# Optimization experiments

Measured on AMD Instinct MI355X. Metric: run time of the kernel, lower is better.

Reference implementation:

```python
import jax, jax.numpy as jnp
import numpy as np
import math

B, S, D = 2, 1024, 512
H = 8
DH = D // H
N_NEURONS = 512
K = 16
N_BASIS = 8
RANK = 64
D_FF = 2048
LN_EPS = 1e-5


def _layer_norm(x, g, b):
    mu = jnp.mean(x, axis=-1, keepdims=True)
    var = jnp.var(x, axis=-1, keepdims=True)
    return (x - mu) * jax.lax.rsqrt(var + LN_EPS) * g + b


def setup_inputs() -> dict:
    key = jax.random.key(0)
    ks = jax.random.split(key, 16)
    x = jax.random.normal(ks[0], (B, S, D), dtype=jnp.float32)
    # causal mask [B,1,S,S] (True = keep)
    mask = jnp.broadcast_to(jnp.tril(jnp.ones((S, S), dtype=bool)), (B, 1, S, S))
    inp = {
        "x": x,
        "neuron_emb": jax.random.normal(ks[1], (N_NEURONS, D)) * 0.02,
        "Wq": jax.random.normal(ks[2], (D, D)) * 0.02, "bq": jnp.zeros((D,)),
        "Wk": jax.random.normal(ks[3], (D, D)) * 0.02, "bk": jnp.zeros((D,)),
        "Wv": jax.random.normal(ks[4], (D, D)) * 0.02, "bv": jnp.zeros((D,)),
        "Wg": jax.random.normal(ks[5], (2 * D, 2)) * 0.02, "bg": jnp.zeros((2,)),
        "basis_A": jax.random.normal(ks[6], (N_BASIS, D, RANK)) * 0.05,
        "basis_B": jax.random.normal(ks[7], (N_BASIS, RANK, D_FF)) * 0.05,
        "neuron_coords": jax.random.normal(ks[8], (N_NEURONS, N_BASIS)) * 0.5,
        "Wd": jax.random.normal(ks[9], (D_FF, D)) * 0.02, "bd": jnp.zeros((D,)),
        "ln1_g": jnp.ones((D,)), "ln1_b": jnp.zeros((D,)),
        "ln2_g": jnp.ones((D,)), "ln2_b": jnp.zeros((D,)),
        "mask": mask,
    }
    return inp


def reference(x, neuron_emb, Wq, bq, Wk, bk, Wv, bv, Wg, bg, basis_A, basis_B,
              neuron_coords, Wd, bd, ln1_g, ln1_b, ln2_g, ln2_b, mask):
    normed = _layer_norm(x, ln1_g, ln1_b)
    # --- router: cross-attention context ---
    q = (normed @ Wq + bq).reshape(B, S, H, DH).transpose(0, 2, 1, 3)
    k = (normed @ Wk + bk).reshape(B, S, H, DH).transpose(0, 2, 1, 3)
    v = (normed @ Wv + bv).reshape(B, S, H, DH).transpose(0, 2, 1, 3)
    attn = jnp.einsum('bhsd,bhtd->bhst', q, k) / math.sqrt(DH)
    attn = jnp.where(mask, attn, -jnp.inf)
    attn = jax.nn.softmax(attn, axis=-1)
    context = jnp.einsum('bhst,bhtd->bhsd', attn, v)
    context = context.transpose(0, 2, 1, 3).reshape(B, S, D)
    # --- gated neuron scoring + top-k ---
    token_scores = normed @ neuron_emb.T            # [B,S,N]
    context_scores = context @ neuron_emb.T         # [B,S,N]
    gate = jax.nn.softmax(jnp.concatenate([normed, context], axis=-1) @ Wg + bg, axis=-1)
    scores = gate[:, :, 0:1] * token_scores + gate[:, :, 1:2] * context_scores
    topk_scores, topk_idx = jax.lax.top_k(scores, K)  # [B,S,K]
    weights = jax.nn.softmax(topk_scores, axis=-1)
    # --- neuron info residual ---
    neuron_info = jnp.einsum('bsk,bskd->bsd', weights, neuron_emb[topk_idx])
    x = x + neuron_info
    # --- per-token basis-mixed low-rank FFN ---
    normed2 = _layer_norm(x, ln2_g, ln2_b)
    coords = neuron_coords[topk_idx]                # [B,S,K,n_basis]
    token_coords = jnp.einsum('bsk,bskn->bsn', weights, coords)  # [B,S,n_basis]
    # h = x @ (sum_n c_n A_n): contract without materializing [B,S,D,R]
    h = jnp.einsum('bsnr,bsn->bsr', jnp.einsum('bsd,ndr->bsnr', normed2, basis_A), token_coords)
    h = jnp.einsum('bsnf,bsn->bsf', jnp.einsum('bsr,nrf->bsnf', h, basis_B), token_coords)
    h = jax.nn.gelu(h, approximate=False)
    out = h @ Wd + bd
    x = x + out
    return (x, topk_idx)
```

## Files before the change

kernel.cpp:

```cpp
#include <hip/hip_runtime.h>
#include <hip/hip_bf16.h>

#define Bv 2
#define Sv 1024
#define Dv 512
#define Hv 8
#define Nv 512
#define Kv 16
#define NBv 8
#define DFv 2048
#define NTOK (Bv*Sv)

typedef __attribute__((ext_vector_type(8))) short short8;
typedef __attribute__((ext_vector_type(4))) float float4v;

__launch_bounds__(256)
__global__ void ln64_k(const float* __restrict__ x, const float* __restrict__ g,
                       const float* __restrict__ b, double* __restrict__ out)
{
    const int t = blockIdx.x;
    const size_t base = (size_t)t * Dv;
    const int tid = threadIdx.x;
    double v0 = (double)x[base + tid];
    double v1 = (double)x[base + tid + 256];
    double s = v0 + v1, ss = v0 * v0 + v1 * v1;
    #pragma unroll
    for (int off = 32; off; off >>= 1) { s += __shfl_xor(s, off); ss += __shfl_xor(ss, off); }
    __shared__ double red[4][2];
    const int wv = tid >> 6, ln = tid & 63;
    if (ln == 0) { red[wv][0] = s; red[wv][1] = ss; }
    __syncthreads();
    s  = red[0][0] + red[1][0] + red[2][0] + red[3][0];
    ss = red[0][1] + red[1][1] + red[2][1] + red[3][1];
    double mu  = s * (1.0 / Dv);
    double var = ss * (1.0 / Dv) - mu * mu;
    double rstd = 1.0 / sqrt(var + 1e-5);
    out[base + tid]       = (v0 - mu) * rstd * (double)g[tid]       + (double)b[tid];
    out[base + tid + 256] = (v1 - mu) * rstd * (double)g[tid + 256] + (double)b[tid + 256];
}

__launch_bounds__(256)
__global__ void qkv64_k(const double* __restrict__ A,
                        const float* __restrict__ Wq, const float* __restrict__ Wk,
                        const float* __restrict__ Wv, const float* __restrict__ bq,
                        const float* __restrict__ bk, const float* __restrict__ bvv,
                        double* __restrict__ qo, double* __restrict__ ko,
                        double* __restrict__ vo)
{
    const int z = blockIdx.z;
    const float* Bm  = (z == 0) ? Wq : (z == 1) ? Wk : Wv;
    const float* bia = (z == 0) ? bq : (z == 1) ? bk : bvv;
    double* Cout     = (z == 0) ? qo : (z == 1) ? ko : vo;
    const int N = Dv, Kd = Dv;
    __shared__ double As[16][68];
    __shared__ double Bs[16][68];
    const int tid = threadIdx.x;
    const int m0 = blockIdx.y * 64, n0 = blockIdx.x * 64;
    const int tx = tid & 15, ty = tid >> 4;
    double acc[4][4] = {};
    const int lm = tid >> 2, lk4 = (tid & 3) << 2;
    for (int k0 = 0; k0 < Kd; k0 += 16) {
        double4 av = *(const double4*)(A + (size_t)(m0 + lm) * Kd + k0 + lk4);
        As[lk4 + 0][lm] = av.x; As[lk4 + 1][lm] = av.y;
        As[lk4 + 2][lm] = av.z; As[lk4 + 3][lm] = av.w;
        const int kk = tid >> 4, n4 = (tid & 15) << 2;
        float4 bv4 = *(const float4*)(Bm + (size_t)(k0 + kk) * N + n0 + n4);
        Bs[kk][n4 + 0] = (double)bv4.x; Bs[kk][n4 + 1] = (double)bv4.y;
        Bs[kk][n4 + 2] = (double)bv4.z; Bs[kk][n4 + 3] = (double)bv4.w;
        __syncthreads();
        #pragma unroll
        for (int kk2 = 0; kk2 < 16; kk2++) {
            double a_[4], b_[4];
            *(double4*)a_ = *(const double4*)&As[kk2][ty << 2];
            *(double4*)b_ = *(const double4*)&Bs[kk2][tx << 2];
            #pragma unroll
            for (int i = 0; i < 4; i++)
                #pragma unroll
                for (int j = 0; j < 4; j++)
                    acc[i][j] = fma(a_[i], b_[j], acc[i][j]);
        }
        __syncthreads();
    }
    #pragma unroll
    for (int i = 0; i < 4; i++) {
        const int row = m0 + (ty << 2) + i;
        #pragma unroll
        for (int j = 0; j < 4; j++) {
            const int col = n0 + (tx << 2) + j;
            Cout[(size_t)row * N + col] = acc[i][j] + (double)bia[col];
        }
    }
}

__launch_bounds__(256)
__global__ void scores64_k(const double* __restrict__ A0, const double* __restrict__ A1,
                           const double* __restrict__ gate, const float* __restrict__ Bm,
                           double* __restrict__ Cbase)
{
    const int M = NTOK, N = Nv, Kd = Dv;
    const int z = blockIdx.z;
    const int kbeg = z * (Dv / 2), kend = kbeg + Dv / 2;
    double* Cout = Cbase + (size_t)z * M * N;
    __shared__ double As[16][68];
    __shared__ double Bs[16][68];
    const int tid = threadIdx.x;
    const int m0 = blockIdx.y * 64, n0 = blockIdx.x * 64;
    const int tx = tid & 15, ty = tid >> 4;
    double acc[4][4] = {};
    const int lm = tid >> 2, lk4 = (tid & 3) << 2;
    for (int k0 = kbeg; k0 < kend; k0 += 16) {
        const double g0 = gate[2 * (m0 + lm)], g1 = gate[2 * (m0 + lm) + 1];
        double4 a0 = *(const double4*)(A0 + (size_t)(m0 + lm) * Kd + k0 + lk4);
        double4 a1 = *(const double4*)(A1 + (size_t)(m0 + lm) * Kd + k0 + lk4);
        As[lk4 + 0][lm] = g0 * a0.x + g1 * a1.x;
        As[lk4 + 1][lm] = g0 * a0.y + g1 * a1.y;
        As[lk4 + 2][lm] = g0 * a0.z + g1 * a1.z;
        As[lk4 + 3][lm] = g0 * a0.w + g1 * a1.w;
        const int nn = tid >> 2, kq = (tid & 3) << 2;
        float4 bv4 = *(const float4*)(Bm + (size_t)(n0 + nn) * Kd + k0 + kq);
        Bs[kq + 0][nn] = (double)bv4.x; Bs[kq + 1][nn] = (double)bv4.y;
        Bs[kq + 2][nn] = (double)bv4.z; Bs[kq + 3][nn] = (double)bv4.w;
        __syncthreads();
        #pragma unroll
        for (int kk = 0; kk < 16; kk++) {
            double a_[4], b_[4];
            *(double4*)a_ = *(const double4*)&As[kk][ty << 2];
            *(double4*)b_ = *(const double4*)&Bs[kk][tx << 2];
            #pragma unroll
            for (int i = 0; i < 4; i++)
                #pragma unroll
                for (int j = 0; j < 4; j++)
                    acc[i][j] = fma(a_[i], b_[j], acc[i][j]);
        }
        __syncthreads();
    }
    #pragma unroll
    for (int i = 0; i < 4; i++) {
        const int row = m0 + (ty << 2) + i;
        #pragma unroll
        for (int j = 0; j < 4; j++)
            Cout[(size_t)row * N + n0 + (tx << 2) + j] = acc[i][j];
    }
}

template<int EPI>
__launch_bounds__(256)
__global__ void mfma_k(const __hip_bfloat16* __restrict__ A, const __hip_bfloat16* __restrict__ B,
                       void* __restrict__ Cout_, int M, int N, int Kt, int kper)
{
    __shared__ __hip_bfloat16 As[128][40];
    __shared__ __hip_bfloat16 Bs[128][40];
    const int tid = threadIdx.x;
    const int m0 = blockIdx.y * 128, n0 = blockIdx.x * 128;
    const int z = blockIdx.z;
    const int kbeg = z * kper, kend = kbeg + kper;
    const int w = tid >> 6, l = tid & 63;
    const int wr = (w >> 1) * 64, wc = (w & 1) * 64;
    const int lm = l & 15, quad = l >> 4;
    float4v acc[4][4];
    #pragma unroll
    for (int i = 0; i < 4; i++)
        #pragma unroll
        for (int j = 0; j < 4; j++)
            acc[i][j] = (float4v){0.f, 0.f, 0.f, 0.f};
    const int srow = tid >> 1, skb = (tid & 1) * 16;
    for (int k0 = kbeg; k0 < kend; k0 += 32) {
        *(uint4*)&As[srow][skb]     = *(const uint4*)(A + (size_t)(m0 + srow) * Kt + k0 + skb);
        *(uint4*)&As[srow][skb + 8] = *(const uint4*)(A + (size_t)(m0 + srow) * Kt + k0 + skb + 8);
        *(uint4*)&Bs[srow][skb]     = *(const uint4*)(B + (size_t)(n0 + srow) * Kt + k0 + skb);
        *(uint4*)&Bs[srow][skb + 8] = *(const uint4*)(B + (size_t)(n0 + srow) * Kt + k0 + skb + 8);
        __syncthreads();
        short8 af[4], bf[4];
        #pragma unroll
        for (int mi = 0; mi < 4; mi++) af[mi] = *(const short8*)&As[wr + mi * 16 + lm][quad * 8];
        #pragma unroll
        for (int ni = 0; ni < 4; ni++) bf[ni] = *(const short8*)&Bs[wc + ni * 16 + lm][quad * 8];
        #pragma unroll
        for (int mi = 0; mi < 4; mi++)
            #pragma unroll
            for (int ni = 0; ni < 4; ni++)
                acc[mi][ni] = __builtin_amdgcn_mfma_f32_16x16x32_bf16(af[mi], bf[ni], acc[mi][ni], 0, 0, 0);
        __syncthreads();
    }
    #pragma unroll
    for (int mi = 0; mi < 4; mi++) {
        #pragma unroll
        for (int ni = 0; ni < 4; ni++) {
            const int col = n0 + wc + ni * 16 + lm;
            #pragma unroll
            for (int r = 0; r < 4; r++) {
                const int row = m0 + wr + mi * 16 + quad * 4 + r;
                float c = acc[mi][ni][r];
                if (EPI == 0) {
                    ((float*)Cout_)[(size_t)z * M * N + (size_t)row * N + col] = c;
                } else {
                    c = 0.5f * c * (1.0f + erff(c * 0.70710678118654752f));
                    ((__hip_bfloat16*)Cout_)[(size_t)row * N + col] = __float2bfloat16(c);
                }
            }
        }
    }
}

__device__ __constant__ int c_slotbase[4] = {0, 0, 384, 640};
__device__ __constant__ int c_cnt[4]      = {0, 24, 16, 8};

__launch_bounds__(256)
__global__ void attn64c_k(const double* __restrict__ q, const double* __restrict__ k,
                          const double* __restrict__ v, double* __restrict__ ctxun,
                          double* __restrict__ Opart, double* __restrict__ mbuf,
                          double* __restrict__ lbuf)
{
    const int qt = blockIdx.x, bh = blockIdx.y, ch = blockIdx.z;
    if (qt < ch * 8) return;
    const int b = bh >> 3, h = bh & 7;
    __shared__ double Qs[32][70];
    __shared__ double Kt[64][34];
    __shared__ double Vs[32][70];
    const int tid = threadIdx.x;
    const int r = tid >> 3, cc = tid & 7;
    const int lane = tid & 63;
    const int lbase = lane & 56;
    const size_t qoff = ((size_t)b * Sv + (size_t)qt * 32) * Dv + h * 64;
    #pragma unroll
    for (int i = 0; i < 4; i++) {
        int f = i * 256 + tid;
        int row = f >> 5, c2 = (f & 31) * 2;
        *(double2*)&Qs[row][c2] = *(const double2*)(q + qoff + (size_t)row * Dv + c2);
    }
    double O[8] = {};
    double mrun = -1e300, lrun = 0.0;
    const int iglob = qt * 32 + r;
    const int jbeg = ch * 8;
    const int jend = (qt < jbeg + 7) ? qt : (jbeg + 7);
    for (int jt = jbeg; jt <= jend; jt++) {
        __syncthreads();
        const size_t koff = ((size_t)b * Sv + (size_t)jt * 32) * Dv + h * 64;
        #pragma unroll
        for (int i = 0; i < 4; i++) {
            int f = i * 256 + tid;
            int row = f >> 5, c2 = (f & 31) * 2;
            double2 kv = *(const double2*)(k + koff + (size_t)row * Dv + c2);
            Kt[c2][row]     = kv.x;
            Kt[c2 + 1][row] = kv.y;
            *(double2*)&Vs[row][c2] = *(const double2*)(v + koff + (size_t)row * Dv + c2);
        }
        __syncthreads();
        double a[4] = {0.0, 0.0, 0.0, 0.0};
        #pragma unroll 8
        for (int kk = 0; kk < 64; kk += 2) {
            double2 qv  = *(const double2*)&Qs[r][kk];
            double2 ka0 = *(const double2*)&Kt[kk][cc * 4];
            double2 ka1 = *(const double2*)&Kt[kk][cc * 4 + 2];
            double2 kb0 = *(const double2*)&Kt[kk + 1][cc * 4];
            double2 kb1 = *(const double2*)&Kt[kk + 1][cc * 4 + 2];
            a[0] = fma(qv.x, ka0.x, fma(qv.y, kb0.x, a[0]));
            a[1] = fma(qv.x, ka0.y, fma(qv.y, kb0.y, a[1]));
            a[2] = fma(qv.x, ka1.x, fma(qv.y, kb1.x, a[2]));
            a[3] = fma(qv.x, ka1.y, fma(qv.y, kb1.y, a[3]));
        }
        double p[4];
        double mx = -1e300;
        #pragma unroll
        for (int jj = 0; jj < 4; jj++) {
            const int jglob = jt * 32 + cc * 4 + jj;
            p[jj] = (jglob <= iglob) ? a[jj] * 0.125 : -1e300;
            mx = fmax(mx, p[jj]);
        }
        mx = fmax(mx, __shfl_xor(mx, 1));
        mx = fmax(mx, __shfl_xor(mx, 2));
        mx = fmax(mx, __shfl_xor(mx, 4));
        const double mnew = fmax(mrun, mx);
        double rsum = 0.0;
        #pragma unroll
        for (int jj = 0; jj < 4; jj++) { p[jj] = exp(p[jj] - mnew); rsum += p[jj]; }
        rsum += __shfl_xor(rsum, 1);
        rsum += __shfl_xor(rsum, 2);
        rsum += __shfl_xor(rsum, 4);
        const double alpha = exp(mrun - mnew);
        lrun = lrun * alpha + rsum;
        mrun = mnew;
        #pragma unroll
        for (int c = 0; c < 8; c++) O[c] *= alpha;
        #pragma unroll
        for (int jsrc = 0; jsrc < 8; jsrc++) {
            #pragma unroll
            for (int jj = 0; jj < 4; jj++) {
                const double pj = __shfl(p[jj], lbase + jsrc);
                const double* vrow = &Vs[jsrc * 4 + jj][cc * 8];
                #pragma unroll
                for (int c2 = 0; c2 < 8; c2 += 2) {
                    double2 vv = *(const double2*)&vrow[c2];
                    O[c2 + 0] = fma(pj, vv.x, O[c2 + 0]);
                    O[c2 + 1] = fma(pj, vv.y, O[c2 + 1]);
                }
            }
        }
    }
    if (cc == 0) {
        const int mi = ((bh * 32 + qt) * 4 + ch) * 32 + r;
        mbuf[mi] = mrun; lbuf[mi] = lrun;
    }
    if (ch == 0) {
        const size_t obase = ((size_t)b * Sv + (size_t)iglob) * Dv + h * 64 + cc * 8;
        #pragma unroll
        for (int c2 = 0; c2 < 8; c2 += 2) { double2 t{O[c2], O[c2+1]}; *(double2*)(ctxun + obase + c2) = t; }
    } else {
        const int slot = c_slotbase[ch] + bh * c_cnt[ch] + (qt - ch * 8);
        const size_t obase = ((size_t)slot * 32 + r) * 64 + cc * 8;
        #pragma unroll
        for (int c2 = 0; c2 < 8; c2 += 2) { double2 t{O[c2], O[c2+1]}; *(double2*)(Opart + obase + c2) = t; }
    }
}

__launch_bounds__(256)
__global__ void attnmerge_k(double* __restrict__ ctx, const double* __restrict__ Opart,
                            const double* __restrict__ mbuf, const double* __restrict__ lbuf)
{
    const size_t i = (size_t)blockIdx.x * 256 + threadIdx.x;
    const size_t e = i * 2;
    const int d = (int)(e & 511);
    const int s = (int)((e >> 9) & 1023);
    const int b = (int)(e >> 19);
    const int h = d >> 6;
    const int qt = s >> 5, r = s & 31;
    const int bh = b * 8 + h;
    int nch = qt >> 3; if (nch > 3) nch = 3;
    const int mib = ((bh * 32 + qt) * 4) * 32 + r;
    double ms = mbuf[mib];
    for (int c = 1; c <= nch; c++) ms = fmax(ms, mbuf[mib + c * 32]);
    double2 o = *(const double2*)(ctx + e);
    double a0 = exp(mbuf[mib] - ms);
    double den = lbuf[mib] * a0;
    o.x *= a0; o.y *= a0;
    for (int c = 1; c <= nch; c++) {
        const double ac = exp(mbuf[mib + c * 32] - ms);
        den += lbuf[mib + c * 32] * ac;
        const int slot = c_slotbase[c] + bh * c_cnt[c] + (qt - c * 8);
        const size_t op = ((size_t)slot * 32 + r) * 64 + (d & 63);
        double2 oc = *(const double2*)(Opart + op);
        o.x = fma(ac, oc.x, o.x);
        o.y = fma(ac, oc.y, o.y);
    }
    const double inv = 1.0 / den;
    o.x *= inv; o.y *= inv;
    *(double2*)(ctx + e) = o;
}

__launch_bounds__(256)
__global__ void gate64_k(const double* __restrict__ normed, const double* __restrict__ ctx,
                         const float* __restrict__ Wg, const float* __restrict__ bg,
                         double* __restrict__ gate)
{
    const int wv = threadIdx.x >> 6, lane = threadIdx.x & 63;
    const int t = blockIdx.x * 4 + wv;
    double a0 = 0.0, a1 = 0.0;
    for (int d = lane; d < Dv; d += 64) {
        double nv = normed[(size_t)t * Dv + d];
        double cv = ctx[(size_t)t * Dv + d];
        a0 += nv * (double)Wg[2 * d]     + cv * (double)Wg[2 * (d + Dv)];
        a1 += nv * (double)Wg[2 * d + 1] + cv * (double)Wg[2 * (d + Dv) + 1];
    }
    #pragma unroll
    for (int off = 32; off; off >>= 1) { a0 += __shfl_xor(a0, off); a1 += __shfl_xor(a1, off); }
    if (lane == 0) {
        a0 += (double)bg[0]; a1 += (double)bg[1];
        double m = fmax(a0, a1);
        double e0 = exp(a0 - m), e1 = exp(a1 - m);
        double inv = 1.0 / (e0 + e1);
        gate[2 * t] = e0 * inv; gate[2 * t + 1] = e1 * inv;
    }
}

__launch_bounds__(256)
__global__ void topk64_k(const double* __restrict__ s0, const float* __restrict__ x,
                         const float* __restrict__ emb, const float* __restrict__ coords,
                         const float* __restrict__ g2, const float* __restrict__ b2,
                         float* __restrict__ x2, __hip_bfloat16* __restrict__ normed2bf,
                         float* __restrict__ tcoords, float* __restrict__ idx_out)
{
    __shared__ double sc[4][Nv];
    const int wv = threadIdx.x >> 6, lane = threadIdx.x & 63;
    const int t = blockIdx.x * 4 + wv;
    const double* s1 = s0 + (size_t)NTOK * Nv;
    double* s = sc[wv];
    #pragma unroll
    for (int i = 0; i < 8; i++) {
        const size_t idx = (size_t)t * Nv + i * 64 + lane;
        s[i * 64 + lane] = s0[idx] + s1[idx];
    }
    __syncthreads();
    double wval[Kv]; int widx[Kv];
    for (int kk = 0; kk < Kv; kk++) {
        double bvv = -1e300; int bi = Nv;
        #pragma unroll
        for (int i = 0; i < 8; i++) {
            const int d = lane * 8 + i;
            const double vv = s[d];
            if (vv > bvv) { bvv = vv; bi = d; }
        }
        #pragma unroll
        for (int off = 1; off < 64; off <<= 1) {
            double ov = __shfl_xor(bvv, off);
            int    oi = __shfl_xor(bi, off);
            if (ov > bvv || (ov == bvv && oi < bi)) { bvv = ov; bi = oi; }
        }
        wval[kk] = bvv; widx[kk] = bi;
        __syncthreads();
        if (lane == (bi >> 3)) s[bi] = -1e301;
        __syncthreads();
        if (lane == kk) idx_out[(size_t)t * Kv + kk] = (float)bi;
    }
    double w[Kv]; double sum = 0.0;
    #pragma unroll
    for (int kk = 0; kk < Kv; kk++) { w[kk] = exp(wval[kk] - wval[0]); sum += w[kk]; }
    const double invs = 1.0 / sum;
    #pragma unroll
    for (int kk = 0; kk < Kv; kk++) w[kk] *= invs;
    float xv[8];
    float sm = 0.0f, sq = 0.0f;
    #pragma unroll
    for (int i = 0; i < 8; i++) {
        const int d = lane + 64 * i;
        double info = 0.0;
        #pragma unroll
        for (int kk = 0; kk < Kv; kk++)
            info = fma(w[kk], (double)emb[(size_t)widx[kk] * Dv + d], info);
        float vv = (float)((double)x[(size_t)t * Dv + d] + info);
        xv[i] = vv;
        x2[(size_t)t * Dv + d] = vv;
        sm += vv; sq += vv * vv;
    }
    #pragma unroll
    for (int off = 32; off; off >>= 1) { sm += __shfl_xor(sm, off); sq += __shfl_xor(sq, off); }
    const float mu = sm * (1.0f / Dv);
    const float var = sq * (1.0f / Dv) - mu * mu;
    const float rstd = rsqrtf(var + 1e-5f);
    #pragma unroll
    for (int i = 0; i < 8; i++) {
        const int d = lane + 64 * i;
        normed2bf[(size_t)t * Dv + d] = __float2bfloat16((xv[i] - mu) * rstd * g2[d] + b2[d]);
    }
    if (lane < NBv) {
        double tc = 0.0;
        #pragma unroll
        for (int kk = 0; kk < Kv; kk++)
            tc = fma(w[kk], (double)coords[(size_t)widx[kk] * NBv + lane], tc);
        tcoords[t * NBv + lane] = (float)tc;
    }
}

__launch_bounds__(256)
__global__ void acatbf_k(const float* __restrict__ bA, __hip_bfloat16* __restrict__ AcatT)
{
    const int i = blockIdx.x * 256 + threadIdx.x;
    const int d = i & 511, nc = i >> 9;
    const int n = nc >> 6, r = nc & 63;
    AcatT[i] = __float2bfloat16(bA[n * 32768 + d * 64 + r]);
}

__launch_bounds__(256)
__global__ void tr2bf_k(const float* __restrict__ in, __hip_bfloat16* __restrict__ out,
                        int R, int C)
{
    __shared__ float tile[32][33];
    const int c0 = blockIdx.x * 32, r0 = blockIdx.y * 32;
    const int tx = threadIdx.x & 31, ty = threadIdx.x >> 5;
    #pragma unroll
    for (int i = 0; i < 4; i++)
        tile[ty + 8 * i][tx] = in[(size_t)(r0 + ty + 8 * i) * C + c0 + tx];
    __syncthreads();
    #pragma unroll
    for (int i = 0; i < 4; i++)
        out[(size_t)(c0 + ty + 8 * i) * R + r0 + tx] = __float2bfloat16(tile[tx][ty + 8 * i]);
}

__launch_bounds__(256)
__global__ void combine_k(const float* __restrict__ Gp, const float* __restrict__ tcoords,
                          __hip_bfloat16* __restrict__ u_bf)
{
    const size_t M1 = (size_t)NTOK * Dv;
    const int wv = threadIdx.x >> 6, lane = threadIdx.x & 63;
    const int t = blockIdx.x * 4 + wv;
    float cs[NBv];
    #pragma unroll
    for (int n = 0; n < NBv; n++) cs[n] = tcoords[t * NBv + n];
    float h = 0.0f;
    #pragma unroll
    for (int n = 0; n < NBv; n++) {
        const size_t gi = (size_t)t * Dv + n * 64 + lane;
        float g = Gp[gi] + Gp[gi + M1] + Gp[gi + 2 * M1] + Gp[gi + 3 * M1];
        h = fmaf(cs[n], g, h);
    }
    #pragma unroll
    for (int n = 0; n < NBv; n++)
        u_bf[(size_t)t * Dv + n * 64 + lane] = __float2bfloat16(cs[n] * h);
}

__launch_bounds__(256)
__global__ void reduce4_k(const float* __restrict__ p4, const float* __restrict__ bd,
                          const float* __restrict__ x2, float* __restrict__ xout)
{
    const size_t M1 = (size_t)NTOK * Dv;
    const size_t i = (size_t)blockIdx.x * 256 + threadIdx.x;
    float c = p4[i] + p4[i + M1] + p4[i + 2 * M1] + p4[i + 3 * M1];
    xout[i] = c + bd[i & 511] + x2[i];
}

extern "C" void kernel_launch(void* const* d_in, const int* in_sizes, int n_in,
                              void* d_out, int out_size, void* d_ws, size_t ws_size,
                              hipStream_t stream) {
    (void)in_sizes; (void)n_in; (void)out_size; (void)ws_size;
    const size_t M1 = (size_t)NTOK * Dv;

    const float* x   = (const float*)d_in[0];
    const float* emb = (const float*)d_in[1];
    const float* Wq  = (const float*)d_in[2];
    const float* bq  = (const float*)d_in[3];
    const float* Wk  = (const float*)d_in[4];
    const float* bk  = (const float*)d_in[5];
    const float* Wv  = (const float*)d_in[6];
    const float* bvv = (const float*)d_in[7];
    const float* Wg  = (const float*)d_in[8];
    const float* bg  = (const float*)d_in[9];
    const float* bA  = (const float*)d_in[10];
    const float* bB  = (const float*)d_in[11];
    const float* crd = (const float*)d_in[12];
    const float* Wd  = (const float*)d_in[13];
    const float* bd  = (const float*)d_in[14];
    const float* l1g = (const float*)d_in[15];
    const float* l1b = (const float*)d_in[16];
    const float* l2g = (const float*)d_in[17];
    const float* l2b = (const float*)d_in[18];

    double* normed64 = (double*)d_ws;
    double* q64      = normed64 + M1;
    double* k64      = q64 + M1;
    double* v64      = k64 + M1;
    double* ctx64    = v64 + M1;
    double* Opart    = ctx64 + M1;
    double* mbuf     = Opart + 1572864;
    double* lbuf     = mbuf + 65536;
    double* gate64   = lbuf + 65536;
    float*  tcoords  = (float*)(gate64 + 4096);
    __hip_bfloat16* AcatT = (__hip_bfloat16*)(tcoords + 16384);

    double* s0 = q64;
    float*  x2 = (float*)v64;
    __hip_bfloat16* normed2bf = (__hip_bfloat16*)(x2 + M1);
    __hip_bfloat16* u_bf      = normed2bf + M1;
    float* Gp = (float*)q64;
    float* p4 = (float*)q64;
    __hip_bfloat16* hf_bf = (__hip_bfloat16*)Opart;
    __hip_bfloat16* bBT   = hf_bf + 4 * M1;
    __hip_bfloat16* WdT   = bBT + M1;

    float* xout    = (float*)d_out;
    float* idx_out = (float*)d_out + M1;

    ln64_k<<<NTOK, 256, 0, stream>>>(x, l1g, l1b, normed64);
    qkv64_k<<<dim3(8, 32, 3), 256, 0, stream>>>(normed64, Wq, Wk, Wv, bq, bk, bvv, q64, k64, v64);
    attn64c_k<<<dim3(32, 16, 4), 256, 0, stream>>>(q64, k64, v64, ctx64, Opart, mbuf, lbuf);
    attnmerge_k<<<(int)(M1 / 512), 256, 0, stream>>>(ctx64, Opart, mbuf, lbuf);
    gate64_k<<<NTOK / 4, 256, 0, stream>>>(normed64, ctx64, Wg, bg, gate64);
    scores64_k<<<dim3(8, 32, 2), 256, 0, stream>>>(normed64, ctx64, gate64, emb, s0);
    topk64_k<<<NTOK / 4, 256, 0, stream>>>(s0, x, emb, crd, l2g, l2b, x2, normed2bf, tcoords, idx_out);
    acatbf_k<<<1024, 256, 0, stream>>>(bA, AcatT);
    tr2bf_k<<<dim3(DFv / 32, Dv / 32), 256, 0, stream>>>(bB, bBT, Dv, DFv);
    tr2bf_k<<<dim3(Dv / 32, DFv / 32), 256, 0, stream>>>(Wd, WdT, DFv, Dv);
    mfma_k<0><<<dim3(4, 16, 4), 256, 0, stream>>>(normed2bf, AcatT, Gp, NTOK, Dv, Dv, Dv / 4);
    combine_k<<<NTOK / 4, 256, 0, stream>>>(Gp, tcoords, u_bf);
    mfma_k<1><<<dim3(16, 16, 1), 256, 0, stream>>>(u_bf, bBT, hf_bf, NTOK, DFv, Dv, Dv);
    mfma_k<0><<<dim3(4, 16, 4), 256, 0, stream>>>(hf_bf, WdT, p4, NTOK, Dv, DFv, DFv / 4);
    reduce4_k<<<(int)(M1 / 256), 256, 0, stream>>>(p4, bd, x2, xout);
}
```

Baseline: 620.8 us.

## Use FP64 MFMA for fused QKV projection with runtime layout probing

Replaces the scalar-FMA FP64 QKV GEMM (three separate z-slices) with one kernel that computes Q, K and V together from a shared A tile. It uses the 16x16x4 f64 MFMA instruction. The kernel first probes the MFMA operand and output lane layout at runtime with known integer inputs and picks a matching mapping. If no mapping matches, it falls back to a scalar FMA path. This aims to move the FP64 GEMM onto matrix cores and to reuse the A tile across all three weights, at the cost of a small probe per block and extra branching.

```diff
diff --git a/kernel.cpp b/kernel.cpp
--- a/kernel.cpp
+++ b/kernel.cpp
@@ -13,6 +13,7 @@
 
 typedef __attribute__((ext_vector_type(8))) short short8;
 typedef __attribute__((ext_vector_type(4))) float float4v;
+typedef __attribute__((ext_vector_type(4))) double dbl4;
 
 __launch_bounds__(256)
 __global__ void ln64_k(const float* __restrict__ x, const float* __restrict__ g,
@@ -40,54 +41,150 @@
 }
 
 __launch_bounds__(256)
-__global__ void qkv64_k(const double* __restrict__ A,
+__global__ void qkvMC_k(const double* __restrict__ A,
                         const float* __restrict__ Wq, const float* __restrict__ Wk,
                         const float* __restrict__ Wv, const float* __restrict__ bq,
                         const float* __restrict__ bk, const float* __restrict__ bvv,
                         double* __restrict__ qo, double* __restrict__ ko,
                         double* __restrict__ vo)
 {
-    const int z = blockIdx.z;
-    const float* Bm  = (z == 0) ? Wq : (z == 1) ? Wk : Wv;
-    const float* bia = (z == 0) ? bq : (z == 1) ? bk : bvv;
-    double* Cout     = (z == 0) ? qo : (z == 1) ? ko : vo;
-    const int N = Dv, Kd = Dv;
-    __shared__ double As[16][68];
-    __shared__ double Bs[16][68];
+    __shared__ double As[32][18];
+    __shared__ double Bs[3][16][66];
     const int tid = threadIdx.x;
-    const int m0 = blockIdx.y * 64, n0 = blockIdx.x * 64;
-    const int tx = tid & 15, ty = tid >> 4;
-    double acc[4][4] = {};
-    const int lm = tid >> 2, lk4 = (tid & 3) << 2;
-    for (int k0 = 0; k0 < Kd; k0 += 16) {
-        double4 av = *(const double4*)(A + (size_t)(m0 + lm) * Kd + k0 + lk4);
-        As[lk4 + 0][lm] = av.x; As[lk4 + 1][lm] = av.y;
-        As[lk4 + 2][lm] = av.z; As[lk4 + 3][lm] = av.w;
-        const int kk = tid >> 4, n4 = (tid & 15) << 2;
-        float4 bv4 = *(const float4*)(Bm + (size_t)(k0 + kk) * N + n0 + n4);
-        Bs[kk][n4 + 0] = (double)bv4.x; Bs[kk][n4 + 1] = (double)bv4.y;
-        Bs[kk][n4 + 2] = (double)bv4.z; Bs[kk][n4 + 3] = (double)bv4.w;
-        __syncthreads();
-        #pragma unroll
-        for (int kk2 = 0; kk2 < 16; kk2++) {
-            double a_[4], b_[4];
-            *(double4*)a_ = *(const double4*)&As[kk2][ty << 2];
-            *(double4*)b_ = *(const double4*)&Bs[kk2][tx << 2];
-            #pragma unroll
-            for (int i = 0; i < 4; i++)
+    const int n0 = blockIdx.x * 64, m0 = blockIdx.y * 32;
+    const int w = tid >> 6, l = tid & 63;
+    const int mt = (w >> 1) * 16, wc = (w & 1) * 32;
+    const int ar = tid >> 3, ak = (tid & 7) * 2;
+    const int bkk = tid >> 4, bn = (tid & 15) * 4;
+
+    int rA = 0, kA = 0, kB = 0, cB = 0, dsel = -1;
+    #pragma unroll 1
+    for (int ab = 0; ab < 4; ab++) {
+        if (dsel >= 0) break;
+        const int a_ = ab & 1, b_ = ab >> 1;
+        const int rA_ = a_ ? (l >> 2) : (l & 15);
+        const int kA_ = a_ ? (l & 3)  : (l >> 4);
+        const int kB_ = b_ ? (l & 3)  : (l >> 4);
+        const int cB_ = b_ ? (l >> 2) : (l & 15);
+        const double av  = (double)(((rA_ * 37 + kA_ * 11) % 19) + 1);
+        const double bvp = (double)(((kB_ * 23 + cB_ * 7) % 17) + 1);
+        dbl4 dd = __builtin_amdgcn_mfma_f64_16x16x4f64(av, bvp, (dbl4){0.0, 0.0, 0.0, 0.0}, 0, 0, 0);
+        #pragma unroll 1
+        for (int d = 0; d < 4; d++) {
+            if (dsel >= 0) break;
+            int okv = 1;
+            #pragma unroll
+            for (int r = 0; r < 4; r++) {
+                const int i_ = (d == 0) ? 4 * (l >> 4) + r
+                             : (d == 1) ? (l & 15)
+                             : (d == 2) ? (l >> 4) + 4 * r
+                             :            (l & 15);
+                const int j_ = (d == 0) ? (l & 15)
+                             : (d == 1) ? 4 * (l >> 4) + r
+                             : (d == 2) ? (l & 15)
+                             :            (l >> 4) + 4 * r;
+                double e = 0.0;
                 #pragma unroll
-                for (int j = 0; j < 4; j++)
-                    acc[i][j] = fma(a_[i], b_[j], acc[i][j]);
-        }
-        __syncthreads();
-    }
-    #pragma unroll
-    for (int i = 0; i < 4; i++) {
-        const int row = m0 + (ty << 2) + i;
-        #pragma unroll
-        for (int j = 0; j < 4; j++) {
-            const int col = n0 + (tx << 2) + j;
-            Cout[(size_t)row * N + col] = acc[i][j] + (double)bia[col];
+                for (int kk2 = 0; kk2 < 4; kk2++)
+                    e += (double)(((i_ * 37 + kk2 * 11) % 19) + 1)
+                       * (double)(((kk2 * 23 + j_ * 7) % 17) + 1);
+                okv &= (dd[r] == e) ? 1 : 0;
+            }
+            if (__all(okv)) { dsel = d; rA = rA_; kA = kA_; kB = kB_; cB = cB_; }
+        }
+    }
+
+    auto stage = [&](int k0) {
+        double2 avv = *(const double2*)(A + (size_t)(m0 + ar) * Dv + k0 + ak);
+        *(double2*)&As[ar][ak] = avv;
+        {
+            float4 b4 = *(const float4*)(Wq + (size_t)(k0 + bkk) * Dv + n0 + bn);
+            Bs[0][bkk][bn] = (double)b4.x; Bs[0][bkk][bn + 1] = (double)b4.y;
+            Bs[0][bkk][bn + 2] = (double)b4.z; Bs[0][bkk][bn + 3] = (double)b4.w;
+        }
+        {
+            float4 b4 = *(const float4*)(Wk + (size_t)(k0 + bkk) * Dv + n0 + bn);
+            Bs[1][bkk][bn] = (double)b4.x; Bs[1][bkk][bn + 1] = (double)b4.y;
+            Bs[1][bkk][bn + 2] = (double)b4.z; Bs[1][bkk][bn + 3] = (double)b4.w;
+        }
+        {
+            float4 b4 = *(const float4*)(Wv + (size_t)(k0 + bkk) * Dv + n0 + bn);
+            Bs[2][bkk][bn] = (double)b4.x; Bs[2][bkk][bn + 1] = (double)b4.y;
+            Bs[2][bkk][bn + 2] = (double)b4.z; Bs[2][bkk][bn + 3] = (double)b4.w;
+        }
+    };
+
+    if (dsel >= 0) {
+        dbl4 acc[3][2];
+        #pragma unroll
+        for (int z = 0; z < 3; z++)
+            #pragma unroll
+            for (int nt = 0; nt < 2; nt++)
+                acc[z][nt] = (dbl4){0.0, 0.0, 0.0, 0.0};
+        for (int k0 = 0; k0 < Dv; k0 += 16) {
+            __syncthreads();
+            stage(k0);
+            __syncthreads();
+            #pragma unroll
+            for (int s = 0; s < 4; s++) {
+                const double aA = As[mt + rA][4 * s + kA];
+                #pragma unroll
+                for (int z = 0; z < 3; z++) {
+                    const double b0 = Bs[z][4 * s + kB][wc + cB];
+                    const double b1 = Bs[z][4 * s + kB][wc + 16 + cB];
+                    acc[z][0] = __builtin_amdgcn_mfma_f64_16x16x4f64(aA, b0, acc[z][0], 0, 0, 0);
+                    acc[z][1] = __builtin_amdgcn_mfma_f64_16x16x4f64(aA, b1, acc[z][1], 0, 0, 0);
+                }
+            }
+        }
+        #pragma unroll
+        for (int r = 0; r < 4; r++) {
+            const int i_ = (dsel == 0) ? 4 * (l >> 4) + r
+                         : (dsel == 1) ? (l & 15)
+                         : (dsel == 2) ? (l >> 4) + 4 * r
+                         :               (l & 15);
+            const int j_ = (dsel == 0) ? (l & 15)
+                         : (dsel == 1) ? 4 * (l >> 4) + r
+                         : (dsel == 2) ? (l & 15)
+                         :               (l >> 4) + 4 * r;
+            const int rowg = m0 + mt + i_;
+            #pragma unroll
+            for (int nt = 0; nt < 2; nt++) {
+                const int colg = n0 + wc + nt * 16 + j_;
+                qo[(size_t)rowg * Dv + colg] = acc[0][nt][r] + (double)bq[colg];
+                ko[(size_t)rowg * Dv + colg] = acc[1][nt][r] + (double)bk[colg];
+                vo[(size_t)rowg * Dv + colg] = acc[2][nt][r] + (double)bvv[colg];
+            }
+        }
+    } else {
+        double fac[3][8];
+        #pragma unroll
+        for (int z = 0; z < 3; z++)
+            #pragma unroll
+            for (int c = 0; c < 8; c++) fac[z][c] = 0.0;
+        const int frow = mt + (l & 15);
+        const int fcb  = wc + (l >> 4) * 8;
+        for (int k0 = 0; k0 < Dv; k0 += 16) {
+            __syncthreads();
+            stage(k0);
+            __syncthreads();
+            #pragma unroll
+            for (int kk = 0; kk < 16; kk++) {
+                const double a = As[frow][kk];
+                #pragma unroll
+                for (int z = 0; z < 3; z++)
+                    #pragma unroll
+                    for (int c = 0; c < 8; c++)
+                        fac[z][c] = fma(a, Bs[z][kk][fcb + c], fac[z][c]);
+            }
+        }
+        const int rowg = m0 + frow;
+        #pragma unroll
+        for (int c = 0; c < 8; c++) {
+            const int colg = n0 + fcb + c;
+            qo[(size_t)rowg * Dv + colg] = fac[0][c] + (double)bq[colg];
+            ko[(size_t)rowg * Dv + colg] = fac[1][c] + (double)bk[colg];
+            vo[(size_t)rowg * Dv + colg] = fac[2][c] + (double)bvv[colg];
         }
     }
 }
@@ -559,7 +656,7 @@
     float* idx_out = (float*)d_out + M1;
 
     ln64_k<<<NTOK, 256, 0, stream>>>(x, l1g, l1b, normed64);
-    qkv64_k<<<dim3(8, 32, 3), 256, 0, stream>>>(normed64, Wq, Wk, Wv, bq, bk, bvv, q64, k64, v64);
+    qkvMC_k<<<dim3(8, 64), 256, 0, stream>>>(normed64, Wq, Wk, Wv, bq, bk, bvv, q64, k64, v64);
     attn64c_k<<<dim3(32, 16, 4), 256, 0, stream>>>(q64, k64, v64, ctx64, Opart, mbuf, lbuf);
     attnmerge_k<<<(int)(M1 / 512), 256, 0, stream>>>(ctx64, Opart, mbuf, lbuf);
     gate64_k<<<NTOK / 4, 256, 0, stream>>>(normed64, ctx64, Wg, bg, gate64);
```

Result: no change. 610.3 us (-1.7%).
